# Performance work log

Hardware: AMD Instinct MI355X
Metric: run time of the kernel (lower is better)

## Reference

```python
import jax, jax.numpy as jnp
import numpy as np
from jax import lax

B, CIN, COUT, H, W = 4, 256, 256, 64, 64
K, DG, STRIDE, PAD, DIL = 3, 1, 1, 1, 1
K2 = K * K
CG = CIN // DG
HO = (H + 2 * PAD - DIL * (K - 1) - 1) // STRIDE + 1
WO = (W + 2 * PAD - DIL * (K - 1) - 1) // STRIDE + 1


def setup_inputs() -> dict:
    key = jax.random.key(0)
    k1, k2, k3 = jax.random.split(key, 3)
    inputs = jax.random.normal(k1, (B, CIN, H, W), jnp.float32)
    # original init_offset() zeros these; small random weights instead so offsets ~0.5px
    w_off = jax.random.normal(k2, (3 * DG * K2, CIN, K, K), jnp.float32) * 0.01
    b_off = jnp.zeros((3 * DG * K2,), jnp.float32)
    w_dcn = jax.random.normal(k3, (COUT, CIN, K, K), jnp.float32) * (1.0 / np.sqrt(CIN * K2))
    b_dcn = jnp.zeros((COUT,), jnp.float32)
    return {"inputs": inputs, "w_off": w_off, "b_off": b_off, "w_dcn": w_dcn, "b_dcn": b_dcn}


def _conv2d(x, w, b):
    y = lax.conv_general_dilated(x, w, (STRIDE, STRIDE), [(PAD, PAD), (PAD, PAD)],
                                 rhs_dilation=(DIL, DIL),
                                 dimension_numbers=("NCHW", "OIHW", "NCHW"))
    return y + b[None, :, None, None]


def _dcn_forward(inputs, w_off, b_off, w_dcn, b_dcn):
    # offset/mask branch (standard conv), then chunk into o1, o2, mask
    om = _conv2d(inputs, w_off, b_off)                      # [B, 3*DG*K2, HO, WO]
    o1, o2, m = jnp.split(om, 3, axis=1)
    offset = jnp.concatenate([o1, o2], axis=1)              # [B, 2*DG*K2, HO, WO]
    mask = jax.nn.sigmoid(m)                                # [B, DG*K2, HO, WO]

    # DCNv2 offset layout: per deformable group, K2 taps of (dy, dx)
    off = offset.reshape(B, DG, K2, 2, HO, WO)
    dy, dx = off[:, :, :, 0], off[:, :, :, 1]               # [B, DG, K2, HO, WO]

    taps = jnp.arange(K2)
    ki = (taps // K).astype(jnp.float32)
    kj = (taps % K).astype(jnp.float32)
    hb = (jnp.arange(HO, dtype=jnp.float32) * STRIDE - PAD)
    wb = (jnp.arange(WO, dtype=jnp.float32) * STRIDE - PAD)
    py = dy + hb[None, None, None, :, None] + (ki * DIL)[None, None, :, None, None]
    px = dx + wb[None, None, None, None, :] + (kj * DIL)[None, None, :, None, None]

    y0f, x0f = jnp.floor(py), jnp.floor(px)
    ly, lx = py - y0f, px - x0f
    y0, x0 = y0f.astype(jnp.int32), x0f.astype(jnp.int32)
    y1, x1 = y0 + 1, x0 + 1

    flat = inputs.reshape(B, DG, CG, H * W)

    def corner(yi, xi, wgt):
        valid = (yi >= 0) & (yi < H) & (xi >= 0) & (xi < W)
        yc = jnp.clip(yi, 0, H - 1)
        xc = jnp.clip(xi, 0, W - 1)
        idx = (yc * W + xc).reshape(B, DG, 1, K2 * HO * WO)
        idx = jnp.broadcast_to(idx, (B, DG, CG, K2 * HO * WO))
        v = jnp.take_along_axis(flat, idx, axis=3).reshape(B, DG, CG, K2, HO, WO)
        w = jnp.where(valid, wgt, 0.0)[:, :, None]          # zero outside (zero-pad bilinear)
        return v * w

    val = (corner(y0, x0, (1 - ly) * (1 - lx)) + corner(y0, x1, (1 - ly) * lx)
           + corner(y1, x0, ly * (1 - lx)) + corner(y1, x1, ly * lx))

    cols = val * mask.reshape(B, DG, 1, K2, HO, WO)         # modulated columns
    cols = cols.reshape(B, CIN * K2, HO * WO)
    out = jnp.einsum("ok,bkn->bon", w_dcn.reshape(COUT, CIN * K2), cols)
    out = out + b_dcn[None, :, None]
    return out.reshape(B, COUT, HO, WO)


def reference(inputs, w_off, b_off, w_dcn, b_dcn):
    return _dcn_forward(inputs, w_off, b_off, w_dcn, b_dcn)
```

## Files before the change

### kernel.cpp

```cpp
#include <hip/hip_runtime.h>
#include <hip/hip_bf16.h>

typedef __bf16 bf16x8 __attribute__((ext_vector_type(8)));
typedef __bf16 bf16x4 __attribute__((ext_vector_type(4)));
typedef float f32x4 __attribute__((ext_vector_type(4)));
typedef unsigned int u32x4 __attribute__((ext_vector_type(4)));

#define CIN 256
#define COUT 256
#define KDIM 2304

__device__ __forceinline__ void gload_lds16(const void* g, void* l) {
  __builtin_amdgcn_global_load_lds(
      (__attribute__((address_space(1))) unsigned int*)g,
      (__attribute__((address_space(3))) unsigned int*)l, 16, 0, 0);
}

__global__ __launch_bounds__(256) void k_prep_all(const float* __restrict__ wdcn,
                                                  const float* __restrict__ woff,
                                                  const float* __restrict__ in,
                                                  __bf16* __restrict__ Ag,
                                                  __bf16* __restrict__ Ah,
                                                  __bf16* __restrict__ Al,
                                                  __bf16* __restrict__ inT) {
  int bid = blockIdx.x, tid = threadIdx.x;
  if (bid < 288) {
    int t8 = bid * 256 + tid;
    int cout = t8 / 288;
    int r8 = t8 - cout * 288;
    int tap = r8 >> 5;
    int cin0 = (r8 & 31) << 3;
    bf16x8 vv;
#pragma unroll
    for (int j = 0; j < 8; ++j)
      vv[j] = (__bf16)wdcn[(cout * 256 + cin0 + j) * 9 + tap];
    *(bf16x8*)&Ag[t8 << 3] = vv;
  } else if (bid < 324) {
    int t8 = (bid - 288) * 256 + tid;
    int l = t8 & 63;
    int mh = (t8 >> 6) & 1;
    int s = t8 >> 7;
    int tap = s >> 3, cc = s & 7;
    int ki = tap / 3, kj = tap - ki * 3;
    int oc = mh * 16 + (l & 15);
    int cinb = cc * 32 + ((l >> 4) << 3);
    bf16x8 hv, lv;
#pragma unroll
    for (int j = 0; j < 8; ++j) {
      float v = (oc < 27) ? woff[((oc * 256 + cinb + j) * 3 + ki) * 3 + kj] : 0.f;
      __bf16 hi = (__bf16)v;
      hv[j] = hi;
      lv[j] = (__bf16)(v - (float)hi);
    }
    *(bf16x8*)&Ah[t8 << 3] = hv;
    *(bf16x8*)&Al[t8 << 3] = lv;
  } else {
    int idx = bid - 324;
    int h = idx & 63, b = idx >> 6;
    int c = tid;
    const float* src = in + ((((b << 8) + c) << 6) + h) * 64;
    __bf16* dst = inT + (((b << 12) + (h << 6)) << 8) + c;
#pragma unroll
    for (int w4 = 0; w4 < 16; ++w4) {
      f32x4 v = *(const f32x4*)(src + (w4 << 2));
#pragma unroll
      for (int k = 0; k < 4; ++k) dst[(((w4 << 2) + k)) << 8] = (__bf16)v[k];
    }
  }
}

__global__ __launch_bounds__(256) void k_conv(const __bf16* __restrict__ inT,
                                              const __bf16* __restrict__ Ah,
                                              const __bf16* __restrict__ Al,
                                              float* __restrict__ omp) {
  __shared__ __bf16 xh[3 * 4 * 66 * 8];
  __shared__ __bf16 sW[2 * 9 * 1024];
  int tid = threadIdx.x;
  int l = tid & 63, wn = tid >> 6;
  int ho = blockIdx.x, b = blockIdx.y, ct = blockIdx.z;

  f32x4 acc[2];
  acc[0] = (f32x4){0.f, 0.f, 0.f, 0.f};
  acc[1] = (f32x4){0.f, 0.f, 0.f, 0.f};

  for (int chunk = 0; chunk < 4; ++chunk) {
    int cin0 = ct * 128 + chunk * 32;
    int scc = ct * 4 + chunk;
    u32x4* sW4 = (u32x4*)sW;
#pragma unroll
    for (int i = 0; i < 9; ++i) {
      int s = i * 256 + tid;
      int a = s / 1152;
      int r = s - a * 1152;
      int tap = r >> 7, w = r & 127;
      const __bf16* src =
          (a ? Al : Ah) + (((tap * 8 + scc) * 2) << 9) + (w << 3);
      gload_lds16((const void*)src, (void*)&sW4[i * 256 + (tid & ~63)]);
    }
    for (int i = tid; i < 792; i += 256) {
      int c = i % 66;
      int t2 = i / 66;
      int u = t2 & 3, r = t2 >> 2;
      int h = ho - 1 + r, w = c - 1;
      bool ok = ((unsigned)h < 64u) & ((unsigned)w < 64u);
      bf16x8 hv = (bf16x8){};
      if (ok)
        hv = *(const bf16x8*)(inT + ((((b << 12) + (h << 6) + w)) << 8) + cin0 +
                              (u << 3));
      *(bf16x8*)&xh[((r * 4 + u) * 66 + c) << 3] = hv;
    }
    __syncthreads();
#pragma unroll
    for (int tap = 0; tap < 9; ++tap) {
      int ki = tap / 3, kj = tap - ki * 3;
      bf16x8 ah0 = *(const bf16x8*)&sW[tap * 1024 + (l << 3)];
      bf16x8 ah1 = *(const bf16x8*)&sW[tap * 1024 + 512 + (l << 3)];
      bf16x8 al0 = *(const bf16x8*)&sW[9216 + tap * 1024 + (l << 3)];
      bf16x8 al1 = *(const bf16x8*)&sW[9216 + tap * 1024 + 512 + (l << 3)];
      int u = l >> 4;
      int sc = (wn << 4) + (l & 15) + kj;
      bf16x8 bh = *(const bf16x8*)&xh[((ki * 4 + u) * 66 + sc) << 3];
      acc[0] = __builtin_amdgcn_mfma_f32_16x16x32_bf16(ah0, bh, acc[0], 0, 0, 0);
      acc[1] = __builtin_amdgcn_mfma_f32_16x16x32_bf16(ah1, bh, acc[1], 0, 0, 0);
      acc[0] = __builtin_amdgcn_mfma_f32_16x16x32_bf16(al0, bh, acc[0], 0, 0, 0);
      acc[1] = __builtin_amdgcn_mfma_f32_16x16x32_bf16(al1, bh, acc[1], 0, 0, 0);
    }
    __syncthreads();
  }
  int n = (ho << 6) + (wn << 4) + (l & 15);
#pragma unroll
  for (int mh = 0; mh < 2; ++mh)
#pragma unroll
    for (int r = 0; r < 4; ++r) {
      int oc = mh * 16 + ((l >> 4) << 2) + r;
      if (oc < 27)
        omp[(((ct * 4 + b) * 27 + oc) << 12) + n] = acc[mh][r];
    }
}

__global__ __launch_bounds__(512, 4) void k_gemm(const __bf16* __restrict__ inT,
                                                 const float* __restrict__ omp,
                                                 const float* __restrict__ boff,
                                                 const __bf16* __restrict__ Ag,
                                                 const float* __restrict__ bdcn,
                                                 float* __restrict__ out) {
  __shared__ u32x4 sA[2048];
  __shared__ u32x4 sB[256];
  int tid = threadIdx.x;
  int l = tid & 63;
  int w = tid >> 6;
  int wm = w & 3, wh = w >> 2;
  int id = blockIdx.x;
  int x = id & 7, t = id >> 3;
  int b = x >> 1;
  int ntile = ((x & 1) << 6) + t;
  int sn = tid >> 4;
  int sc = tid & 15;
  int n_g = (ntile << 5) + sn;
  const __bf16* tb = inT + ((b << 12) << 8);

  f32x4 acc[4];
#pragma unroll
  for (int i = 0; i < 4; ++i) acc[i] = (f32x4){0.f, 0.f, 0.f, 0.f};

  float w00 = 0.f, w01 = 0.f, w10 = 0.f, w11 = 0.f;
  int o00 = 0, o01 = 0, o10 = 0, o11 = 0;

  for (int step = 0; step < 36; ++step) {
    int tap = step >> 2;
    int cin0 = (step & 3) << 6;
    if ((step & 3) == 0) {
      int ki = tap / 3, kj = tap - ki * 3;
      float dy = omp[((b * 27 + 2 * tap) << 12) + n_g] +
                 omp[(((4 + b) * 27 + 2 * tap) << 12) + n_g] + boff[2 * tap];
      float dx = omp[((b * 27 + 2 * tap + 1) << 12) + n_g] +
                 omp[(((4 + b) * 27 + 2 * tap + 1) << 12) + n_g] + boff[2 * tap + 1];
      float mv = omp[((b * 27 + 18 + tap) << 12) + n_g] +
                 omp[(((4 + b) * 27 + 18 + tap) << 12) + n_g] + boff[18 + tap];
      float msk = 1.f / (1.f + __expf(-mv));
      float py = dy + (float)((n_g >> 6) - 1 + ki);
      float px = dx + (float)((n_g & 63) - 1 + kj);
      float y0f = floorf(py), x0f = floorf(px);
      float ly = py - y0f, lx = px - x0f;
      int y0 = (int)y0f, x0 = (int)x0f;
      int y1 = y0 + 1, x1 = x0 + 1;
      bool vy0 = (y0 >= 0) & (y0 < 64), vy1 = (y1 >= 0) & (y1 < 64);
      bool vx0 = (x0 >= 0) & (x0 < 64), vx1 = (x1 >= 0) & (x1 < 64);
      float hy = 1.f - ly, hx = 1.f - lx;
      w00 = (vy0 & vx0) ? hy * hx * msk : 0.f;
      w01 = (vy0 & vx1) ? hy * lx * msk : 0.f;
      w10 = (vy1 & vx0) ? ly * hx * msk : 0.f;
      w11 = (vy1 & vx1) ? ly * lx * msk : 0.f;
      int y0c = min(max(y0, 0), 63), y1c = min(max(y1, 0), 63);
      int x0c = min(max(x0, 0), 63), x1c = min(max(x1, 0), 63);
      o00 = (y0c << 6) + x0c;
      o01 = (y0c << 6) + x1c;
      o10 = (y1c << 6) + x0c;
      o11 = (y1c << 6) + x1c;
    }
    int cb0 = cin0 + (sc << 2);
    bf16x4 cA = *(const bf16x4*)(tb + (o00 << 8) + cb0);
    bf16x4 cB = *(const bf16x4*)(tb + (o01 << 8) + cb0);
    bf16x4 cC = *(const bf16x4*)(tb + (o10 << 8) + cb0);
    bf16x4 cD = *(const bf16x4*)(tb + (o11 << 8) + cb0);
    bf16x4 vv;
#pragma unroll
    for (int j = 0; j < 4; ++j) {
      vv[j] = (__bf16)(w00 * (float)cA[j] + w01 * (float)cB[j] +
                       w10 * (float)cC[j] + w11 * (float)cD[j]);
    }
    __syncthreads();
    int kk0 = (tap << 8) + cin0;
#pragma unroll
    for (int i = 0; i < 4; ++i) {
      int slot = i * 512 + tid;
      int m = slot >> 3, j = slot & 7;
      int csrc = j ^ (m & 7);
      const __bf16* src = Ag + m * KDIM + kk0 + (csrc << 3);
      gload_lds16((const void*)src, (void*)&sA[i * 512 + (tid & ~63)]);
    }
    {
      unsigned long long* sB64 = (unsigned long long*)sB;
      int slot = (sn << 3) + ((sc >> 1) ^ (sn & 7));
      sB64[slot * 2 + (sc & 1)] = __builtin_bit_cast(unsigned long long, vv);
    }
    __syncthreads();
#pragma unroll
    for (int kt = 0; kt < 2; ++kt) {
      bf16x8 af[4], bfr;
      int cc = (kt << 2) + (l >> 4);
#pragma unroll
      for (int mf = 0; mf < 4; ++mf) {
        int m = (wm << 6) + (mf << 4) + (l & 15);
        af[mf] = __builtin_bit_cast(bf16x8, sA[(m << 3) + (cc ^ (m & 7))]);
      }
      {
        int n = (wh << 4) + (l & 15);
        bfr = __builtin_bit_cast(bf16x8, sB[(n << 3) + (cc ^ (n & 7))]);
      }
#pragma unroll
      for (int mf = 0; mf < 4; ++mf)
        acc[mf] = __builtin_amdgcn_mfma_f32_16x16x32_bf16(af[mf], bfr, acc[mf],
                                                          0, 0, 0);
    }
  }
#pragma unroll
  for (int mf = 0; mf < 4; ++mf)
#pragma unroll
    for (int r = 0; r < 4; ++r) {
      int m = (wm << 6) + (mf << 4) + ((l >> 4) << 2) + r;
      int n = (ntile << 5) + (wh << 4) + (l & 15);
      out[((b * COUT + m) << 12) + n] = acc[mf][r] + bdcn[m];
    }
}

extern "C" void kernel_launch(void* const* d_in, const int* in_sizes, int n_in,
                              void* d_out, int out_size, void* d_ws, size_t ws_size,
                              hipStream_t stream) {
  const float* in = (const float*)d_in[0];
  const float* woff = (const float*)d_in[1];
  const float* boff = (const float*)d_in[2];
  const float* wdcn = (const float*)d_in[3];
  const float* bdcn = (const float*)d_in[4];
  float* out = (float*)d_out;
  char* ws = (char*)d_ws;
  __bf16* Ag = (__bf16*)ws;
  __bf16* Ah = (__bf16*)(ws + 1179648);
  __bf16* Al = (__bf16*)(ws + 1327104);
  float* omp = (float*)(ws + 1474560);
  __bf16* inT = (__bf16*)(ws + 5013504);
  k_prep_all<<<580, 256, 0, stream>>>(wdcn, woff, in, Ag, Ah, Al, inT);
  k_conv<<<dim3(64, 4, 2), 256, 0, stream>>>(inT, Ah, Al, omp);
  k_gemm<<<512, 512, 0, stream>>>(inT, omp, boff, Ag, bdcn, out);
}
```

Before: 82.68 us.

## Drop low-part offset weights and software-pipeline gathers and A loads in GEMM

The offset conv no longer uses a hi/lo bf16 split of the offset weights. It keeps only the bf16 high part, which halves the MFMAs and the LDS weight traffic in k_conv. The main GEMM is restructured so that the bilinear corner gathers and the A-tile loads for the next step go into registers before the current step's MFMAs, then are stored to LDS on the following iteration. This replaces the direct global-to-LDS loads and overlaps memory latency with compute. It costs extra registers and gives up offset precision, which could shift sampling positions slightly.

Result: faster. 79.16 us (-4.3%).

```diff
diff --git a/kernel.cpp b/kernel.cpp
--- a/kernel.cpp
+++ b/kernel.cpp
@@ -21,7 +21,6 @@
                                                   const float* __restrict__ in,
                                                   __bf16* __restrict__ Ag,
                                                   __bf16* __restrict__ Ah,
-                                                  __bf16* __restrict__ Al,
                                                   __bf16* __restrict__ inT) {
   int bid = blockIdx.x, tid = threadIdx.x;
   if (bid < 288) {
@@ -44,16 +43,13 @@
     int ki = tap / 3, kj = tap - ki * 3;
     int oc = mh * 16 + (l & 15);
     int cinb = cc * 32 + ((l >> 4) << 3);
-    bf16x8 hv, lv;
+    bf16x8 hv;
 #pragma unroll
     for (int j = 0; j < 8; ++j) {
       float v = (oc < 27) ? woff[((oc * 256 + cinb + j) * 3 + ki) * 3 + kj] : 0.f;
-      __bf16 hi = (__bf16)v;
-      hv[j] = hi;
-      lv[j] = (__bf16)(v - (float)hi);
+      hv[j] = (__bf16)v;
     }
     *(bf16x8*)&Ah[t8 << 3] = hv;
-    *(bf16x8*)&Al[t8 << 3] = lv;
   } else {
     int idx = bid - 324;
     int h = idx & 63, b = idx >> 6;
@@ -71,10 +67,9 @@
 
 __global__ __launch_bounds__(256) void k_conv(const __bf16* __restrict__ inT,
                                               const __bf16* __restrict__ Ah,
-                                              const __bf16* __restrict__ Al,
                                               float* __restrict__ omp) {
   __shared__ __bf16 xh[3 * 4 * 66 * 8];
-  __shared__ __bf16 sW[2 * 9 * 1024];
+  __shared__ __bf16 sW[9 * 1024];
   int tid = threadIdx.x;
   int l = tid & 63, wn = tid >> 6;
   int ho = blockIdx.x, b = blockIdx.y, ct = blockIdx.z;
@@ -88,14 +83,13 @@
     int scc = ct * 4 + chunk;
     u32x4* sW4 = (u32x4*)sW;
 #pragma unroll
-    for (int i = 0; i < 9; ++i) {
+    for (int i = 0; i < 5; ++i) {
       int s = i * 256 + tid;
-      int a = s / 1152;
-      int r = s - a * 1152;
-      int tap = r >> 7, w = r & 127;
-      const __bf16* src =
-          (a ? Al : Ah) + (((tap * 8 + scc) * 2) << 9) + (w << 3);
-      gload_lds16((const void*)src, (void*)&sW4[i * 256 + (tid & ~63)]);
+      if (s < 1152) {
+        int tap = s >> 7, w = s & 127;
+        const __bf16* src = Ah + (((tap * 8 + scc) * 2) << 9) + (w << 3);
+        gload_lds16((const void*)src, (void*)&sW4[i * 256 + (tid & ~63)]);
+      }
     }
     for (int i = tid; i < 792; i += 256) {
       int c = i % 66;
@@ -115,15 +109,11 @@
       int ki = tap / 3, kj = tap - ki * 3;
       bf16x8 ah0 = *(const bf16x8*)&sW[tap * 1024 + (l << 3)];
       bf16x8 ah1 = *(const bf16x8*)&sW[tap * 1024 + 512 + (l << 3)];
-      bf16x8 al0 = *(const bf16x8*)&sW[9216 + tap * 1024 + (l << 3)];
-      bf16x8 al1 = *(const bf16x8*)&sW[9216 + tap * 1024 + 512 + (l << 3)];
       int u = l >> 4;
       int sc = (wn << 4) + (l & 15) + kj;
       bf16x8 bh = *(const bf16x8*)&xh[((ki * 4 + u) * 66 + sc) << 3];
       acc[0] = __builtin_amdgcn_mfma_f32_16x16x32_bf16(ah0, bh, acc[0], 0, 0, 0);
       acc[1] = __builtin_amdgcn_mfma_f32_16x16x32_bf16(ah1, bh, acc[1], 0, 0, 0);
-      acc[0] = __builtin_amdgcn_mfma_f32_16x16x32_bf16(al0, bh, acc[0], 0, 0, 0);
-      acc[1] = __builtin_amdgcn_mfma_f32_16x16x32_bf16(al1, bh, acc[1], 0, 0, 0);
     }
     __syncthreads();
   }
@@ -165,66 +155,82 @@
 
   float w00 = 0.f, w01 = 0.f, w10 = 0.f, w11 = 0.f;
   int o00 = 0, o01 = 0, o10 = 0, o11 = 0;
-
-  for (int step = 0; step < 36; ++step) {
-    int tap = step >> 2;
-    int cin0 = (step & 3) << 6;
-    if ((step & 3) == 0) {
-      int ki = tap / 3, kj = tap - ki * 3;
-      float dy = omp[((b * 27 + 2 * tap) << 12) + n_g] +
-                 omp[(((4 + b) * 27 + 2 * tap) << 12) + n_g] + boff[2 * tap];
-      float dx = omp[((b * 27 + 2 * tap + 1) << 12) + n_g] +
-                 omp[(((4 + b) * 27 + 2 * tap + 1) << 12) + n_g] + boff[2 * tap + 1];
-      float mv = omp[((b * 27 + 18 + tap) << 12) + n_g] +
-                 omp[(((4 + b) * 27 + 18 + tap) << 12) + n_g] + boff[18 + tap];
-      float msk = 1.f / (1.f + __expf(-mv));
-      float py = dy + (float)((n_g >> 6) - 1 + ki);
-      float px = dx + (float)((n_g & 63) - 1 + kj);
-      float y0f = floorf(py), x0f = floorf(px);
-      float ly = py - y0f, lx = px - x0f;
-      int y0 = (int)y0f, x0 = (int)x0f;
-      int y1 = y0 + 1, x1 = x0 + 1;
-      bool vy0 = (y0 >= 0) & (y0 < 64), vy1 = (y1 >= 0) & (y1 < 64);
-      bool vx0 = (x0 >= 0) & (x0 < 64), vx1 = (x1 >= 0) & (x1 < 64);
-      float hy = 1.f - ly, hx = 1.f - lx;
-      w00 = (vy0 & vx0) ? hy * hx * msk : 0.f;
-      w01 = (vy0 & vx1) ? hy * lx * msk : 0.f;
-      w10 = (vy1 & vx0) ? ly * hx * msk : 0.f;
-      w11 = (vy1 & vx1) ? ly * lx * msk : 0.f;
-      int y0c = min(max(y0, 0), 63), y1c = min(max(y1, 0), 63);
-      int x0c = min(max(x0, 0), 63), x1c = min(max(x1, 0), 63);
-      o00 = (y0c << 6) + x0c;
-      o01 = (y0c << 6) + x1c;
-      o10 = (y1c << 6) + x0c;
-      o11 = (y1c << 6) + x1c;
-    }
-    int cb0 = cin0 + (sc << 2);
-    bf16x4 cA = *(const bf16x4*)(tb + (o00 << 8) + cb0);
-    bf16x4 cB = *(const bf16x4*)(tb + (o01 << 8) + cb0);
-    bf16x4 cC = *(const bf16x4*)(tb + (o10 << 8) + cb0);
-    bf16x4 cD = *(const bf16x4*)(tb + (o11 << 8) + cb0);
-    bf16x4 vv;
-#pragma unroll
-    for (int j = 0; j < 4; ++j) {
-      vv[j] = (__bf16)(w00 * (float)cA[j] + w01 * (float)cB[j] +
-                       w10 * (float)cC[j] + w11 * (float)cD[j]);
-    }
-    __syncthreads();
-    int kk0 = (tap << 8) + cin0;
+  bf16x4 cA, cB, cC, cD;
+  u32x4 ar[4];
+
+  auto do_corners = [&](int tap) {
+    int ki = tap / 3, kj = tap - ki * 3;
+    float dy = omp[((b * 27 + 2 * tap) << 12) + n_g] +
+               omp[(((4 + b) * 27 + 2 * tap) << 12) + n_g] + boff[2 * tap];
+    float dx = omp[((b * 27 + 2 * tap + 1) << 12) + n_g] +
+               omp[(((4 + b) * 27 + 2 * tap + 1) << 12) + n_g] + boff[2 * tap + 1];
+    float mv = omp[((b * 27 + 18 + tap) << 12) + n_g] +
+               omp[(((4 + b) * 27 + 18 + tap) << 12) + n_g] + boff[18 + tap];
+    float msk = 1.f / (1.f + __expf(-mv));
+    float py = dy + (float)((n_g >> 6) - 1 + ki);
+    float px = dx + (float)((n_g & 63) - 1 + kj);
+    float y0f = floorf(py), x0f = floorf(px);
+    float ly = py - y0f, lx = px - x0f;
+    int y0 = (int)y0f, x0 = (int)x0f;
+    int y1 = y0 + 1, x1 = x0 + 1;
+    bool vy0 = (y0 >= 0) & (y0 < 64), vy1 = (y1 >= 0) & (y1 < 64);
+    bool vx0 = (x0 >= 0) & (x0 < 64), vx1 = (x1 >= 0) & (x1 < 64);
+    float hy = 1.f - ly, hx = 1.f - lx;
+    w00 = (vy0 & vx0) ? hy * hx * msk : 0.f;
+    w01 = (vy0 & vx1) ? hy * lx * msk : 0.f;
+    w10 = (vy1 & vx0) ? ly * hx * msk : 0.f;
+    w11 = (vy1 & vx1) ? ly * lx * msk : 0.f;
+    int y0c = min(max(y0, 0), 63), y1c = min(max(y1, 0), 63);
+    int x0c = min(max(x0, 0), 63), x1c = min(max(x1, 0), 63);
+    o00 = (y0c << 6) + x0c;
+    o01 = (y0c << 6) + x1c;
+    o10 = (y1c << 6) + x0c;
+    o11 = (y1c << 6) + x1c;
+  };
+  auto do_gather = [&](int s1) {
+    int cb0 = ((s1 & 3) << 6) + (sc << 2);
+    cA = *(const bf16x4*)(tb + (o00 << 8) + cb0);
+    cB = *(const bf16x4*)(tb + (o01 << 8) + cb0);
+    cC = *(const bf16x4*)(tb + (o10 << 8) + cb0);
+    cD = *(const bf16x4*)(tb + (o11 << 8) + cb0);
+  };
+  auto do_aload = [&](int s1) {
+    int kk0 = s1 << 6;
 #pragma unroll
     for (int i = 0; i < 4; ++i) {
       int slot = i * 512 + tid;
       int m = slot >> 3, j = slot & 7;
       int csrc = j ^ (m & 7);
-      const __bf16* src = Ag + m * KDIM + kk0 + (csrc << 3);
-      gload_lds16((const void*)src, (void*)&sA[i * 512 + (tid & ~63)]);
-    }
+      ar[i] = *(const u32x4*)(Ag + m * KDIM + kk0 + (csrc << 3));
+    }
+  };
+
+  do_corners(0);
+  do_gather(0);
+  do_aload(0);
+
+  for (int step = 0; step < 36; ++step) {
+    bf16x4 vv;
+#pragma unroll
+    for (int j = 0; j < 4; ++j) {
+      vv[j] = (__bf16)(w00 * (float)cA[j] + w01 * (float)cB[j] +
+                       w10 * (float)cC[j] + w11 * (float)cD[j]);
+    }
+    __syncthreads();
+#pragma unroll
+    for (int i = 0; i < 4; ++i) sA[i * 512 + tid] = ar[i];
     {
       unsigned long long* sB64 = (unsigned long long*)sB;
       int slot = (sn << 3) + ((sc >> 1) ^ (sn & 7));
       sB64[slot * 2 + (sc & 1)] = __builtin_bit_cast(unsigned long long, vv);
     }
     __syncthreads();
+    if (step < 35) {
+      int s1 = step + 1;
+      if ((s1 & 3) == 0) do_corners(s1 >> 2);
+      do_gather(s1);
+      do_aload(s1);
+    }
 #pragma unroll
     for (int kt = 0; kt < 2; ++kt) {
       bf16x8 af[4], bfr;
@@ -266,10 +272,9 @@
   char* ws = (char*)d_ws;
   __bf16* Ag = (__bf16*)ws;
   __bf16* Ah = (__bf16*)(ws + 1179648);
-  __bf16* Al = (__bf16*)(ws + 1327104);
   float* omp = (float*)(ws + 1474560);
   __bf16* inT = (__bf16*)(ws + 5013504);
-  k_prep_all<<<580, 256, 0, stream>>>(wdcn, woff, in, Ag, Ah, Al, inT);
-  k_conv<<<dim3(64, 4, 2), 256, 0, stream>>>(inT, Ah, Al, omp);
+  k_prep_all<<<580, 256, 0, stream>>>(wdcn, woff, in, Ag, Ah, inT);
+  k_conv<<<dim3(64, 4, 2), 256, 0, stream>>>(inT, Ah, omp);
   k_gemm<<<512, 512, 0, stream>>>(inT, omp, boff, Ag, bdcn, out);
 }
```

## Drop low-part bf16 split for offset conv weights and vectorize input transpose

Applied to the files above, without the earlier changes.

Removes the hi/lo bf16 split of the offset-branch conv weights, so k_conv does half the MFMAs, stages half the weight LDS and loads half as many weight tiles. The input NCHW-to-NHWC bf16 transpose now has each thread convert an 8x8 channel-by-width block and write 16-byte vectors instead of scattered 2-byte stores. Dropping the low part lowers precision of the offset/mask prediction, which can shift sampling positions and hurt accuracy.

Result: faster. 80.08 us (-3.2%).

```diff
diff --git a/kernel.cpp b/kernel.cpp
--- a/kernel.cpp
+++ b/kernel.cpp
@@ -21,7 +21,6 @@
                                                   const float* __restrict__ in,
                                                   __bf16* __restrict__ Ag,
                                                   __bf16* __restrict__ Ah,
-                                                  __bf16* __restrict__ Al,
                                                   __bf16* __restrict__ inT) {
   int bid = blockIdx.x, tid = threadIdx.x;
   if (bid < 288) {
@@ -44,37 +43,45 @@
     int ki = tap / 3, kj = tap - ki * 3;
     int oc = mh * 16 + (l & 15);
     int cinb = cc * 32 + ((l >> 4) << 3);
-    bf16x8 hv, lv;
+    bf16x8 hv;
 #pragma unroll
     for (int j = 0; j < 8; ++j) {
       float v = (oc < 27) ? woff[((oc * 256 + cinb + j) * 3 + ki) * 3 + kj] : 0.f;
-      __bf16 hi = (__bf16)v;
-      hv[j] = hi;
-      lv[j] = (__bf16)(v - (float)hi);
+      hv[j] = (__bf16)v;
     }
     *(bf16x8*)&Ah[t8 << 3] = hv;
-    *(bf16x8*)&Al[t8 << 3] = lv;
   } else {
     int idx = bid - 324;
     int h = idx & 63, b = idx >> 6;
-    int c = tid;
-    const float* src = in + ((((b << 8) + c) << 6) + h) * 64;
-    __bf16* dst = inT + (((b << 12) + (h << 6)) << 8) + c;
-#pragma unroll
-    for (int w4 = 0; w4 < 16; ++w4) {
-      f32x4 v = *(const f32x4*)(src + (w4 << 2));
-#pragma unroll
-      for (int k = 0; k < 4; ++k) dst[(((w4 << 2) + k)) << 8] = (__bf16)v[k];
+    int cg = tid >> 3;
+    int wg = tid & 7;
+    const float* src = in + (((b << 8) + (cg << 3)) << 12) + (h << 6) + (wg << 3);
+    float vals[8][8];
+#pragma unroll
+    for (int j = 0; j < 8; ++j) {
+      f32x4 lo = *(const f32x4*)(src + (j << 12));
+      f32x4 hi = *(const f32x4*)(src + (j << 12) + 4);
+#pragma unroll
+      for (int k = 0; k < 4; ++k) {
+        vals[j][k] = lo[k];
+        vals[j][4 + k] = hi[k];
+      }
+    }
+#pragma unroll
+    for (int k = 0; k < 8; ++k) {
+      bf16x8 vv;
+#pragma unroll
+      for (int j = 0; j < 8; ++j) vv[j] = (__bf16)vals[j][k];
+      *(bf16x8*)&inT[(((b << 12) + (h << 6) + (wg << 3) + k) << 8) + (cg << 3)] = vv;
     }
   }
 }
 
 __global__ __launch_bounds__(256) void k_conv(const __bf16* __restrict__ inT,
                                               const __bf16* __restrict__ Ah,
-                                              const __bf16* __restrict__ Al,
                                               float* __restrict__ omp) {
   __shared__ __bf16 xh[3 * 4 * 66 * 8];
-  __shared__ __bf16 sW[2 * 9 * 1024];
+  __shared__ __bf16 sW[9 * 1024];
   int tid = threadIdx.x;
   int l = tid & 63, wn = tid >> 6;
   int ho = blockIdx.x, b = blockIdx.y, ct = blockIdx.z;
@@ -88,14 +95,13 @@
     int scc = ct * 4 + chunk;
     u32x4* sW4 = (u32x4*)sW;
 #pragma unroll
-    for (int i = 0; i < 9; ++i) {
+    for (int i = 0; i < 5; ++i) {
       int s = i * 256 + tid;
-      int a = s / 1152;
-      int r = s - a * 1152;
-      int tap = r >> 7, w = r & 127;
-      const __bf16* src =
-          (a ? Al : Ah) + (((tap * 8 + scc) * 2) << 9) + (w << 3);
-      gload_lds16((const void*)src, (void*)&sW4[i * 256 + (tid & ~63)]);
+      if (s < 1152) {
+        int tap = s >> 7, w = s & 127;
+        const __bf16* src = Ah + (((tap * 8 + scc) * 2) << 9) + (w << 3);
+        gload_lds16((const void*)src, (void*)&sW4[i * 256 + (tid & ~63)]);
+      }
     }
     for (int i = tid; i < 792; i += 256) {
       int c = i % 66;
@@ -115,15 +121,11 @@
       int ki = tap / 3, kj = tap - ki * 3;
       bf16x8 ah0 = *(const bf16x8*)&sW[tap * 1024 + (l << 3)];
       bf16x8 ah1 = *(const bf16x8*)&sW[tap * 1024 + 512 + (l << 3)];
-      bf16x8 al0 = *(const bf16x8*)&sW[9216 + tap * 1024 + (l << 3)];
-      bf16x8 al1 = *(const bf16x8*)&sW[9216 + tap * 1024 + 512 + (l << 3)];
       int u = l >> 4;
       int sc = (wn << 4) + (l & 15) + kj;
       bf16x8 bh = *(const bf16x8*)&xh[((ki * 4 + u) * 66 + sc) << 3];
       acc[0] = __builtin_amdgcn_mfma_f32_16x16x32_bf16(ah0, bh, acc[0], 0, 0, 0);
       acc[1] = __builtin_amdgcn_mfma_f32_16x16x32_bf16(ah1, bh, acc[1], 0, 0, 0);
-      acc[0] = __builtin_amdgcn_mfma_f32_16x16x32_bf16(al0, bh, acc[0], 0, 0, 0);
-      acc[1] = __builtin_amdgcn_mfma_f32_16x16x32_bf16(al1, bh, acc[1], 0, 0, 0);
     }
     __syncthreads();
   }
@@ -266,10 +268,9 @@
   char* ws = (char*)d_ws;
   __bf16* Ag = (__bf16*)ws;
   __bf16* Ah = (__bf16*)(ws + 1179648);
-  __bf16* Al = (__bf16*)(ws + 1327104);
   float* omp = (float*)(ws + 1474560);
   __bf16* inT = (__bf16*)(ws + 5013504);
-  k_prep_all<<<580, 256, 0, stream>>>(wdcn, woff, in, Ag, Ah, Al, inT);
-  k_conv<<<dim3(64, 4, 2), 256, 0, stream>>>(inT, Ah, Al, omp);
+  k_prep_all<<<580, 256, 0, stream>>>(wdcn, woff, in, Ag, Ah, inT);
+  k_conv<<<dim3(64, 4, 2), 256, 0, stream>>>(inT, Ah, omp);
   k_gemm<<<512, 512, 0, stream>>>(inT, omp, boff, Ag, bdcn, out);
 }
```
